# Optimization experiments

Hardware: AMD Instinct MI355X
Metric: run time of the kernel (lower is better)

Reference implementation:

```python
import jax, jax.numpy as jnp
import numpy as np

SOC, EOS = 3, 2
NUM_HEADS = 12
LN_EPS = 1e-5


def setup_inputs() -> dict:
    key = jax.random.key(0)
    ks = jax.random.split(key, 24)
    B, S, D, N, FF, K = 8, 4096, 768, 1024, 3072, 640
    img = jax.random.normal(ks[0], (B, N, D), jnp.float32)
    hid = jax.random.normal(ks[1], (B, S, D), jnp.float32)
    seq = jax.random.randint(ks[2], (B, S), 4, 100)
    m = jax.random.uniform(ks[3], (B, S)) < 0.125
    seq = jnp.where(m, SOC, seq).at[:, 0].set(SOC)  # ensure >=1 SOC per row
    w = lambda k, a, b: jax.random.normal(k, (a, b), jnp.float32) * 0.02
    return {
        "img": img, "hid": hid, "seq": seq,
        "wq_s": w(ks[4], D, D), "wk_s": w(ks[5], D, D), "wv_s": w(ks[6], D, D), "wo_s": w(ks[7], D, D),
        "wq_c": w(ks[8], D, D), "wk_c": w(ks[9], D, D), "wv_c": w(ks[10], D, D), "wo_c": w(ks[11], D, D),
        "w_ff1": w(ks[12], D, FF), "w_ff2": w(ks[13], FF, D),
        "ln1_s": jnp.ones((D,)), "ln1_b": jnp.zeros((D,)),
        "ln2_s": jnp.ones((D,)), "ln2_b": jnp.zeros((D,)),
        "ln3_s": jnp.ones((D,)), "ln3_b": jnp.zeros((D,)),
        "cap": K,
    }


def _ln(x, s, b):
    mu = jnp.mean(x, axis=-1, keepdims=True)
    var = jnp.var(x, axis=-1, keepdims=True)
    return (x - mu) * jax.lax.rsqrt(var + LN_EPS) * s + b


def _mha(q_in, kv_in, wq, wk, wv, wo, key_mask):
    # q_in [B,Lq,D], kv_in [B,Lk,D], key_mask [B,Lk] bool or None
    B, Lq, D = q_in.shape
    H = NUM_HEADS
    dh = D // H
    q = (q_in @ wq).reshape(B, Lq, H, dh)
    k = (kv_in @ wk).reshape(B, -1, H, dh)
    v = (kv_in @ wv).reshape(B, -1, H, dh)
    scores = jnp.einsum("bqhd,bkhd->bhqk", q, k) / np.sqrt(dh).astype(q.dtype)
    if key_mask is not None:
        scores = jnp.where(key_mask[:, None, None, :], scores, jnp.asarray(-1e9, scores.dtype))
    att = jax.nn.softmax(scores, axis=-1)
    out = jnp.einsum("bhqk,bkhd->bqhd", att, v).reshape(B, Lq, D)
    return out @ wo


def _extract(data, mask, cap):
    # data [B,S,...], mask [B,S] bool -> packed+zero-padded [B,cap,...]
    pos = jnp.cumsum(mask, axis=1) - 1          # slot for each valid token
    pos = jnp.where(mask, pos, cap)             # invalid tokens -> dump slot
    def one(d, p):
        buf = jnp.zeros((cap + 1,) + d.shape[1:], d.dtype)
        return buf.at[p].set(d)[:cap]
        # note: dump slot cap is sliced away
    return jax.vmap(one)(data, pos), pos


def reference(img, hid, seq, wq_s, wk_s, wv_s, wo_s, wq_c, wk_c, wv_c, wo_c,
              w_ff1, w_ff2, ln1_s, ln1_b, ln2_s, ln2_b, ln3_s, ln3_b, cap):
    # mask: SOC tokens occurring before the first EOS
    soc = (seq == SOC) & (jnp.cumsum(seq == EOS, axis=1) == 0)  # [B,S]
    ext, pos = _extract(hid, soc, cap)                          # [B,K,D]
    counts = jnp.sum(soc, axis=1)                               # [B]
    run = jnp.arange(cap)[None, :] < counts[:, None]            # [B,K] valid slots

    # Blocks: pre-LN self-attn (key mask = run), cross-attn to img, FFN
    x = ext
    x = x + _mha(_ln(x, ln1_s, ln1_b), _ln(x, ln1_s, ln1_b), wq_s, wk_s, wv_s, wo_s, run)
    x = x + _mha(_ln(x, ln2_s, ln2_b), img, wq_c, wk_c, wv_c, wo_c, None)
    h = _ln(x, ln3_s, ln3_b)
    x = x + jax.nn.gelu(h @ w_ff1) @ w_ff2

    # masked_scatter back: each SOC position (b,s) takes x[b, pos[b,s]]
    idx = jnp.clip(pos, 0, cap - 1)
    gathered = jnp.take_along_axis(x, idx[:, :, None], axis=1)  # [B,S,D]
    hid_new = jnp.where(soc[:, :, None], gathered, hid)
    return hid_new, x
```

## Files before the change

### kernel.cpp

```cpp
#include <hip/hip_runtime.h>
#include <hip/hip_bf16.h>


#define B_    8
#define S_    4096
#define D_    768
#define N_    1024
#define FF_   3072
#define H_    12
#define DH_   64
#define KCAP  640
#define SOC_TOK 3
#define EOS_TOK 2

typedef __hip_bfloat16 bf16;
typedef unsigned short u16;
typedef __attribute__((ext_vector_type(8))) short short8;
typedef __attribute__((ext_vector_type(4))) float f32x4;

__device__ __forceinline__ u16 ftou16(float x){ union{bf16 b; u16 s;} c; c.b = __float2bfloat16(x); return c.s; }
__device__ __forceinline__ unsigned pk2(float lo, float hi){ return (unsigned)ftou16(lo) | ((unsigned)ftou16(hi)<<16); }

__device__ __forceinline__ f32x4 MFMA(short8 a, short8 b, f32x4 c){
  return __builtin_amdgcn_mfma_f32_16x16x32_bf16(a, b, c, 0, 0, 0);
}

__device__ __forceinline__ void gld16(const void* gp, void* lp){
  __builtin_amdgcn_global_load_lds(
    reinterpret_cast<const __attribute__((address_space(1))) unsigned int*>((size_t)gp),
    reinterpret_cast<__attribute__((address_space(3))) unsigned int*>((size_t)lp),
    16, 0, 0);
}

template<int N> __device__ __forceinline__ void vwait(){
  asm volatile("s_waitcnt vmcnt(%0)" :: "i"(N) : "memory");
}
__device__ __forceinline__ void wgbar(){ asm volatile("s_barrier" ::: "memory"); }

__device__ __forceinline__ int xcd_swz(){
  int id = blockIdx.x;
  return (id & 7) * ((int)gridDim.x >> 3) + (id >> 3);
}

__device__ void scan_body(const int* __restrict__ seq, int* __restrict__ pos,
                          int* __restrict__ src, int* __restrict__ counts, int b){
  int tid = threadIdx.x;
  __shared__ int sd[256];
  __shared__ int carryE, carryS;
  if (tid==0){ carryE=0; carryS=0; }
  __syncthreads();
  for (int c=0; c<S_; c+=256){
    int s   = c + tid;
    int tok = seq[b*S_ + s];
    int isE = (tok==EOS_TOK) ? 1 : 0;
    int isS = (tok==SOC_TOK) ? 1 : 0;
    sd[tid]=isE; __syncthreads();
    for (int off=1; off<256; off<<=1){ int t_=(tid>=off)?sd[tid-off]:0; __syncthreads(); sd[tid]+=t_; __syncthreads(); }
    int eIncl = sd[tid];
    int eTot  = sd[255];
    int valid = (isS && (carryE + eIncl)==0) ? 1 : 0;
    __syncthreads();
    sd[tid]=valid; __syncthreads();
    for (int off=1; off<256; off<<=1){ int t_=(tid>=off)?sd[tid-off]:0; __syncthreads(); sd[tid]+=t_; __syncthreads(); }
    int vIncl = sd[tid];
    int vTot  = sd[255];
    if (valid){
      int slot = carryS + vIncl - 1;
      pos[b*S_ + s] = slot;
      if (slot < KCAP) src[b*KCAP + slot] = s;
    } else {
      pos[b*S_ + s] = -1;
    }
    __syncthreads();
    if (tid==0){ carryE += eTot; carryS += vTot; }
    __syncthreads();
  }
  if (tid==0) counts[b] = (carryS < KCAP) ? carryS : KCAP;
}

struct TransArgs { const float* w[10]; u16* o[10]; };
__global__ __launch_bounds__(256) void transpose_scan_k(TransArgs a, const int* __restrict__ seq,
                                                        int* __restrict__ pos, int* __restrict__ src,
                                                        int* __restrict__ counts,
                                                        const float* __restrict__ img, u16* __restrict__ imgB){
  int id = blockIdx.x;
  if (id >= 9224){
    int base = (id - 9224)*2048 + threadIdx.x*8;
    float4 a0 = *(const float4*)(img + base);
    float4 a1 = *(const float4*)(img + base + 4);
    uint4 wv;
    wv.x = pk2(a0.x,a0.y); wv.y = pk2(a0.z,a0.w); wv.z = pk2(a1.x,a1.y); wv.w = pk2(a1.z,a1.w);
    *(uint4*)(imgB + base) = wv;
    return;
  }
  if (id >= 9216){ scan_body(seq, pos, src, counts, id - 9216); return; }
  __shared__ float tile[32][33];
  int wi, t, K, N;
  if (id < 4608){ wi = id/576; t = id%576; K = 768; N = 768; }
  else if (id < 6912){ wi = 8; t = id-4608; K = 768; N = 3072; }
  else { wi = 9; t = id-6912; K = 3072; N = 768; }
  const float* in = a.w[wi]; u16* out = a.o[wi];
  int nbx = N >> 5;
  int bx = t % nbx, by = t / nbx;
  int tx = threadIdx.x & 31, ty = threadIdx.x >> 5;
  #pragma unroll
  for (int i=0;i<4;++i)
    tile[ty + i*8][tx] = in[(size_t)(by*32 + ty + i*8)*N + bx*32 + tx];
  __syncthreads();
  #pragma unroll
  for (int i=0;i<4;++i)
    out[(size_t)(bx*32 + ty + i*8)*K + by*32 + tx] = ftou16(tile[tx][ty + i*8]);
}

__global__ __launch_bounds__(256) void gather_ln_k(const float* __restrict__ hid,
                                                   const int* __restrict__ src,
                                                   const int* __restrict__ counts,
                                                   const float* __restrict__ g, const float* __restrict__ bt,
                                                   float* __restrict__ X, u16* __restrict__ T0){
  int bk = blockIdx.x; int b = bk / KCAP; int k = bk % KCAP;
  int tid = threadIdx.x;
  float v0, v1, v2;
  if (k < counts[b]){
    const float* hr = hid + ((size_t)b*S_ + src[b*KCAP + k])*D_;
    v0 = hr[tid]; v1 = hr[tid+256]; v2 = hr[tid+512];
  } else { v0 = v1 = v2 = 0.f; }
  float* xr = X + (size_t)bk*D_;
  xr[tid] = v0; xr[tid+256] = v1; xr[tid+512] = v2;
  float s1=v0+v1+v2, s2=v0*v0+v1*v1+v2*v2;
  for (int off=32; off; off>>=1){ s1+=__shfl_xor(s1,off); s2+=__shfl_xor(s2,off); }
  __shared__ float red[8];
  __shared__ float mu_s, rs_s;
  int w=tid>>6, ln=tid&63;
  if (ln==0){ red[w]=s1; red[4+w]=s2; }
  __syncthreads();
  if (tid==0){
    float S1=red[0]+red[1]+red[2]+red[3];
    float S2=red[4]+red[5]+red[6]+red[7];
    float mu = S1*(1.f/D_);
    float var= S2*(1.f/D_) - mu*mu;
    mu_s=mu; rs_s=rsqrtf(var + 1e-5f);
  }
  __syncthreads();
  float mu=mu_s, rs=rs_s;
  u16* yr = T0 + (size_t)bk*D_;
  yr[tid]     = ftou16((v0-mu)*rs*g[tid]     + bt[tid]);
  yr[tid+256] = ftou16((v1-mu)*rs*g[tid+256] + bt[tid+256]);
  yr[tid+512] = ftou16((v2-mu)*rs*g[tid+512] + bt[tid+512]);
}

__global__ __launch_bounds__(256) void ln_k(const float* __restrict__ X, u16* __restrict__ Y,
                                            const float* __restrict__ g, const float* __restrict__ bt){
  int r = blockIdx.x; int tid = threadIdx.x;
  const float* xr = X + (size_t)r*D_;
  float v0=xr[tid], v1=xr[tid+256], v2=xr[tid+512];
  float s1=v0+v1+v2, s2=v0*v0+v1*v1+v2*v2;
  for (int off=32; off; off>>=1){ s1+=__shfl_xor(s1,off); s2+=__shfl_xor(s2,off); }
  __shared__ float red[8];
  __shared__ float mu_s, rs_s;
  int w=tid>>6, ln=tid&63;
  if (ln==0){ red[w]=s1; red[4+w]=s2; }
  __syncthreads();
  if (tid==0){
    float S1=red[0]+red[1]+red[2]+red[3];
    float S2=red[4]+red[5]+red[6]+red[7];
    float mu = S1*(1.f/D_);
    float var= S2*(1.f/D_) - mu*mu;
    mu_s=mu; rs_s=rsqrtf(var + 1e-5f);
  }
  __syncthreads();
  float mu=mu_s, rs=rs_s;
  u16* yr = Y + (size_t)r*D_;
  yr[tid]     = ftou16((v0-mu)*rs*g[tid]     + bt[tid]);
  yr[tid+256] = ftou16((v1-mu)*rs*g[tid+256] + bt[tid+256]);
  yr[tid+512] = ftou16((v2-mu)*rs*g[tid+512] + bt[tid+512]);
}

template<int MODE, int BM, typename TA>
__device__ __forceinline__ void gemm_body(char* ldsp, const TA* __restrict__ A, const u16* __restrict__ Bt,
                                          void* __restrict__ C0, void* __restrict__ C1, void* __restrict__ C2,
                                          int wgid, int N, int K){
  constexpr int MI   = BM/32;
  constexpr int NBUF = (BM==128) ? 2 : ((sizeof(TA)==4) ? 2 : 3);
  u16* As = (u16*)ldsp;
  u16* Bs = (u16*)(ldsp + NBUF*(BM*32)*2);
  int nbx = N >> 7;
  int bx = wgid % nbx, by = wgid / nbx;
  int tid = threadIdx.x;
  int w = tid>>6, l = tid&63, g = l>>4, c = l&15;
  int wr = w&1, wc = w>>1;
  f32x4 acc[MI][4] = {};
  float4 rg[4];
  const int NK = K/32;

  auto STAGEB = [&](int buf, int kt){
    #pragma unroll
    for (int p=0;p<2;++p){
      int row = w*32 + p*16 + (l>>2);
      int su  = (l&3) ^ ((row>>1)&3);
      gld16((const void*)(Bt + (size_t)(bx*128+row)*K + kt + su*8), (void*)&Bs[buf*128*32 + (w*32+p*16)*32]);
    }
  };
  auto STAGEA16 = [&](int buf, int kt){
    if constexpr (BM==128){
      #pragma unroll
      for (int p=0;p<2;++p){
        int row = w*32 + p*16 + (l>>2);
        int su  = (l&3) ^ ((row>>1)&3);
        gld16((const void*)((const u16*)A + (size_t)(by*BM+row)*K + kt + su*8), (void*)&As[buf*BM*32 + (w*32+p*16)*32]);
      }
    } else {
      int row = w*16 + (l>>2);
      int su  = (l&3) ^ ((row>>1)&3);
      gld16((const void*)((const u16*)A + (size_t)(by*BM+row)*K + kt + su*8), (void*)&As[buf*BM*32 + (w*16)*32]);
    }
  };
  auto LOADREG = [&](int kt){
    if constexpr (BM==128){
      const float* ap = (const float*)A + (size_t)(by*BM + (tid>>1))*K + kt + (tid&1)*16;
      rg[0]=*(const float4*)ap;     rg[1]=*(const float4*)(ap+4);
      rg[2]=*(const float4*)(ap+8); rg[3]=*(const float4*)(ap+12);
    } else {
      const float* ap = (const float*)A + (size_t)(by*BM + (tid>>2))*K + kt + (tid&3)*8;
      rg[0] = *(const float4*)ap; rg[1] = *(const float4*)(ap+4);
    }
  };
  auto WRITEA = [&](int buf){
    if constexpr (BM==128){
      int row = tid>>1, half = tid&1;
      uint4 w0,w1;
      w0.x=pk2(rg[0].x,rg[0].y); w0.y=pk2(rg[0].z,rg[0].w); w0.z=pk2(rg[1].x,rg[1].y); w0.w=pk2(rg[1].z,rg[1].w);
      w1.x=pk2(rg[2].x,rg[2].y); w1.y=pk2(rg[2].z,rg[2].w); w1.z=pk2(rg[3].x,rg[3].y); w1.w=pk2(rg[3].z,rg[3].w);
      int sw = (row>>1)&3;
      *(uint4*)&As[buf*BM*32 + row*32 + ((half*2  )^sw)*8] = w0;
      *(uint4*)&As[buf*BM*32 + row*32 + ((half*2+1)^sw)*8] = w1;
    } else {
      int row = tid>>2, unit = tid&3;
      uint4 wv;
      wv.x=pk2(rg[0].x,rg[0].y); wv.y=pk2(rg[0].z,rg[0].w); wv.z=pk2(rg[1].x,rg[1].y); wv.w=pk2(rg[1].z,rg[1].w);
      int sw = (row>>1)&3;
      *(uint4*)&As[buf*BM*32 + row*32 + (unit^sw)*8] = wv;
    }
  };
  auto COMPUTE = [&](int buf){
    short8 af[MI], bfr[4];
    #pragma unroll
    for (int mi=0;mi<MI;++mi){ int row = wr*(MI*16) + mi*16 + c; af[mi]  = *(const short8*)&As[buf*BM*32 + row*32 + (g^((row>>1)&3))*8]; }
    #pragma unroll
    for (int ni=0;ni<4;++ni){ int row = wc*64 + ni*16 + c;       bfr[ni] = *(const short8*)&Bs[buf*128*32 + row*32 + (g^((row>>1)&3))*8]; }
    #pragma unroll
    for (int mi=0;mi<MI;++mi)
      #pragma unroll
      for (int ni=0;ni<4;++ni) acc[mi][ni] = MFMA(af[mi], bfr[ni], acc[mi][ni]);
  };

  if constexpr (BM==128 || sizeof(TA)==4){
    if constexpr (sizeof(TA)==4){ LOADREG(0); STAGEB(0,0); WRITEA(0); }
    else { STAGEA16(0,0); STAGEB(0,0); }
    __syncthreads();
    int buf = 0;
    for (int t=0;t<NK;++t){
      int ktn = (t+1)*32;
      if constexpr (sizeof(TA)==4){
        if (t+1<NK){ LOADREG(ktn); STAGEB(buf^1, ktn); }
        COMPUTE(buf);
        if (t+1<NK) WRITEA(buf^1);
      } else {
        if (t+1<NK){ STAGEA16(buf^1, ktn); STAGEB(buf^1, ktn); }
        COMPUTE(buf);
      }
      __syncthreads();
      buf ^= 1;
    }
  } else {
    constexpr int LPS = 3;
    STAGEA16(0,0);  STAGEB(0,0);
    STAGEA16(1,32); STAGEB(1,32);
    vwait<LPS>();
    wgbar();
    int buf = 0;
    for (int t=0;t<NK;++t){
      if (t+2 < NK){
        int nb = buf+2; if (nb>=3) nb-=3;
        STAGEA16(nb,(t+2)*32); STAGEB(nb,(t+2)*32);
      }
      COMPUTE(buf);
      if (t < NK-2) vwait<LPS>(); else vwait<0>();
      wgbar();
      ++buf; if (buf==3) buf=0;
    }
  }

  int row0 = by*BM + wr*(MI*16), col0 = bx*128 + wc*64;
  #pragma unroll
  for (int mi=0;mi<MI;++mi)
    #pragma unroll
    for (int ni=0;ni<4;++ni){
      int rowb = row0 + mi*16 + g*4;
      int col  = col0 + ni*16 + c;
      if (MODE==4 && col >= 1536){
        int vv = col - 1536; int bb = rowb / KCAP; int key = rowb - bb*KCAP;
        ushort4 pk;
        pk.x = ftou16(acc[mi][ni][0]); pk.y = ftou16(acc[mi][ni][1]);
        pk.z = ftou16(acc[mi][ni][2]); pk.w = ftou16(acc[mi][ni][3]);
        *(ushort4*)&((u16*)C2)[((size_t)(bb*768 + vv))*KCAP + key] = pk;
      } else if (MODE==5 && col >= 768){
        int vv = col - 768; int bb = rowb >> 10; int key = rowb & 1023;
        ushort4 pk;
        pk.x = ftou16(acc[mi][ni][0]); pk.y = ftou16(acc[mi][ni][1]);
        pk.z = ftou16(acc[mi][ni][2]); pk.w = ftou16(acc[mi][ni][3]);
        *(ushort4*)&((u16*)C2)[((size_t)(bb*768 + vv))*1024 + key] = pk;
      } else {
        #pragma unroll
        for (int r=0;r<4;++r){
          int row = rowb + r;
          float v = acc[mi][ni][r];
          if (MODE==0){
            ((u16*)C0)[(size_t)row*N + col] = ftou16(v);
          } else if (MODE==1){
            ((float*)C0)[(size_t)row*N + col] += v;
          } else if (MODE==2){
            float z2 = 1.5957691216057308f*(v + 0.044715f*v*v*v);
            float e  = __expf(z2);
            float th = 1.f - 2.f/(e + 1.f);
            ((u16*)C0)[(size_t)row*N + col] = ftou16(0.5f*v*(1.f+th));
          } else if (MODE==6){
            size_t idx = (size_t)row*N + col;
            float fin = ((float*)C0)[idx] + v;
            ((float*)C0)[idx] = fin;
            ((float*)C1)[idx] = fin;
          } else if (MODE==4){
            if (col < 768)  ((u16*)C0)[(size_t)row*768 + col]       = ftou16(v);
            else            ((u16*)C1)[(size_t)row*768 + col - 768] = ftou16(v);
          } else {
            ((u16*)C0)[(size_t)row*768 + col] = ftou16(v);
          }
        }
      }
    }
}

template<int MODE, int BM, typename TA>
__global__ __launch_bounds__(256) void gemm_k(const TA* __restrict__ A, const u16* __restrict__ Bt,
                                              void* __restrict__ C0, void* __restrict__ C1, void* __restrict__ C2,
                                              int N, int K){
  constexpr int NBUF = (BM==128) ? 2 : ((sizeof(TA)==4) ? 2 : 3);
  __shared__ __align__(16) char pool[NBUF*(BM+128)*32*2];
  gemm_body<MODE,BM,TA>(pool, A, Bt, C0, C1, C2, xcd_swz(), N, K);
}

__global__ __launch_bounds__(256) void mega1_k(const u16* __restrict__ T0, const u16* __restrict__ wqkv_st,
                                               u16* __restrict__ Qb, u16* __restrict__ Kb, u16* __restrict__ VtS,
                                               const u16* __restrict__ imgB, const u16* __restrict__ wkv_ct,
                                               u16* __restrict__ KbC, u16* __restrict__ VtC){
  __shared__ __align__(16) char pool[2*(128+128)*32*2];
  int wgid = xcd_swz();
  if (wgid < 720) gemm_body<4,128,u16>(pool, T0,   wqkv_st, Qb,  Kb,      VtS, wgid,     2304, 768);
  else            gemm_body<5,128,u16>(pool, imgB, wkv_ct,  KbC, nullptr, VtC, wgid-720, 1536, 768);
}

template<int MASKED>
__global__ __launch_bounds__(256) void attn_k(const u16* __restrict__ Q, const u16* __restrict__ Kb,
                                              const u16* __restrict__ Vt, u16* __restrict__ O,
                                              const int* __restrict__ counts, int Lk){
  __shared__ __align__(16) u16 Ks[3][64*64];
  __shared__ __align__(16) u16 Vs[3][64*64];
  __shared__ __align__(16) u16 P[4][16][72];
  int tid = threadIdx.x;
  int w = tid>>6, l = tid&63, g = l>>4, c = l&15;
  int wgid = xcd_swz();
  int qc = wgid % 5;
  int bh = wgid / 5;
  int h = bh % H_, b = bh / H_;
  int q0 = qc*128 + w*32;
  int cnt = MASKED ? counts[b] : Lk;
  int nt = (cnt + 63) >> 6;

  short8 qf[2][2];
  #pragma unroll
  for (int mi=0;mi<2;++mi){
    const u16* Qrow = Q + ((size_t)(b*KCAP + q0 + mi*16 + c))*D_ + h*DH_;
    qf[mi][0] = *(const short8*)(Qrow + g*8);
    qf[mi][1] = *(const short8*)(Qrow + 32 + g*8);
  }

  int srow8 = (l>>3);
  int sunit = l&7;
  auto STAGE = [&](int buf, int kb){
    #pragma unroll
    for (int p=0;p<2;++p){
      int r0 = w*16 + p*8;
      int rowK = r0 + srow8;
      int su = sunit ^ (rowK&7);
      gld16((const void*)(Kb + ((size_t)(b*Lk + kb + rowK))*D_ + h*DH_ + su*8), (void*)&Ks[buf][r0*64]);
      gld16((const void*)(Vt + ((size_t)(b*D_ + h*DH_ + rowK))*Lk + kb + su*8), (void*)&Vs[buf][r0*64]);
    }
  };

  f32x4 o[2][4] = {};
  float m_[2][4], l_[2][4] = {};
  #pragma unroll
  for (int mi=0;mi<2;++mi)
    #pragma unroll
    for (int r=0;r<4;++r) m_[mi][r] = -1e30f;

  STAGE(0, 0);
  if (nt > 1){ STAGE(1, 64); vwait<4>(); } else { vwait<0>(); }
  wgbar();
  int buf = 0;
  for (int t=0; t<nt; ++t){
    int kb = t*64;
    if (t+2 < nt){
      int nb = buf+2; if (nb>=3) nb-=3;
      STAGE(nb, kb+128);
    }
    short8 fr[4][2];
    #pragma unroll
    for (int nb=0;nb<4;++nb)
      #pragma unroll
      for (int kh=0;kh<2;++kh)
        fr[nb][kh] = *(const short8*)&Ks[buf][(nb*16+c)*64 + (((kh<<2)|g) ^ (c&7))*8];
    f32x4 z[2][4];
    #pragma unroll
    for (int mi=0;mi<2;++mi)
      #pragma unroll
      for (int nb=0;nb<4;++nb){
        f32x4 zz = {0.f,0.f,0.f,0.f};
        zz = MFMA(qf[mi][0], fr[nb][0], zz);
        zz = MFMA(qf[mi][1], fr[nb][1], zz);
        z[mi][nb] = zz;
      }
    float pv[2][4][4];
    #pragma unroll
    for (int nb=0;nb<4;++nb){
      bool msk = MASKED && (kb + nb*16 + c >= cnt);
      #pragma unroll
      for (int mi=0;mi<2;++mi)
        #pragma unroll
        for (int r=0;r<4;++r) pv[mi][nb][r] = msk ? -1e30f : z[mi][nb][r]*0.125f;
    }
    float scl[2][4];
    #pragma unroll
    for (int mi=0;mi<2;++mi){
      #pragma unroll
      for (int r=0;r<4;++r){
        float v = fmaxf(fmaxf(pv[mi][0][r],pv[mi][1][r]), fmaxf(pv[mi][2][r],pv[mi][3][r]));
        v = fmaxf(v, __shfl_xor(v,1)); v = fmaxf(v, __shfl_xor(v,2));
        v = fmaxf(v, __shfl_xor(v,4)); v = fmaxf(v, __shfl_xor(v,8));
        float nm = fmaxf(m_[mi][r], v);
        scl[mi][r] = __expf(m_[mi][r] - nm);
        m_[mi][r] = nm;
      }
      #pragma unroll
      for (int r=0;r<4;++r){
        float acc2 = 0.f;
        #pragma unroll
        for (int nb=0;nb<4;++nb){
          float e = __expf(pv[mi][nb][r] - m_[mi][r]);
          pv[mi][nb][r] = e; acc2 += e;
        }
        acc2 += __shfl_xor(acc2,1); acc2 += __shfl_xor(acc2,2);
        acc2 += __shfl_xor(acc2,4); acc2 += __shfl_xor(acc2,8);
        l_[mi][r] = l_[mi][r]*scl[mi][r] + acc2;
      }
      #pragma unroll
      for (int nbd=0;nbd<4;++nbd)
        #pragma unroll
        for (int r=0;r<4;++r) o[mi][nbd][r] *= scl[mi][r];
    }
    #pragma unroll
    for (int nbd=0;nbd<4;++nbd)
      #pragma unroll
      for (int kh=0;kh<2;++kh)
        fr[nbd][kh] = *(const short8*)&Vs[buf][(nbd*16+c)*64 + (((kh<<2)|g) ^ (c&7))*8];
    #pragma unroll
    for (int mi=0;mi<2;++mi){
      #pragma unroll
      for (int nb=0;nb<4;++nb)
        #pragma unroll
        for (int r=0;r<4;++r) P[w][g*4+r][nb*16+c] = ftou16(pv[mi][nb][r]);
      short8 pa0 = *(const short8*)&P[w][c][g*8];
      short8 pa1 = *(const short8*)&P[w][c][32 + g*8];
      #pragma unroll
      for (int nbd=0;nbd<4;++nbd){
        o[mi][nbd] = MFMA(pa0, fr[nbd][0], o[mi][nbd]);
        o[mi][nbd] = MFMA(pa1, fr[nbd][1], o[mi][nbd]);
      }
    }
    if (t < nt-2) vwait<4>(); else vwait<0>();
    wgbar();
    ++buf; if (buf==3) buf=0;
  }
  #pragma unroll
  for (int mi=0;mi<2;++mi)
    #pragma unroll
    for (int nbd=0;nbd<4;++nbd)
      #pragma unroll
      for (int r=0;r<4;++r)
        O[((size_t)(b*KCAP + q0 + mi*16 + g*4 + r))*D_ + h*DH_ + nbd*16 + c] = ftou16(o[mi][nbd][r] / l_[mi][r]);
}

__global__ __launch_bounds__(256) void scatter_k(const int* __restrict__ pos, const float* __restrict__ X,
                                                 const float* __restrict__ hid, float* __restrict__ out0){
  int bs = blockIdx.x; int tid = threadIdx.x;
  int b = bs >> 12;
  int p = pos[bs];
  float* orow = out0 + (size_t)bs*D_;
  if (p >= 0){
    int pc = p < KCAP ? p : (KCAP-1);
    const float* xr = X + ((size_t)(b*KCAP + pc))*D_;
    orow[tid]     = xr[tid];
    orow[tid+256] = xr[tid+256];
    orow[tid+512] = xr[tid+512];
  } else {
    const float* hr = hid + (size_t)bs*D_;
    orow[tid]     = hr[tid];
    orow[tid+256] = hr[tid+256];
    orow[tid+512] = hr[tid+512];
  }
}

extern "C" void kernel_launch(void* const* d_in, const int* in_sizes, int n_in,
                              void* d_out, int out_size, void* d_ws, size_t ws_size,
                              hipStream_t stream){
  const float* img  = (const float*)d_in[0];
  const float* hid  = (const float*)d_in[1];
  const int*   seq  = (const int*)  d_in[2];
  const float* W[10] = { (const float*)d_in[3], (const float*)d_in[4], (const float*)d_in[5], (const float*)d_in[6],
                         (const float*)d_in[7], (const float*)d_in[8], (const float*)d_in[9], (const float*)d_in[10],
                         (const float*)d_in[11], (const float*)d_in[12] };
  const float* ln1s = (const float*)d_in[13];
  const float* ln1b = (const float*)d_in[14];
  const float* ln2s = (const float*)d_in[15];
  const float* ln2b = (const float*)d_in[16];
  const float* ln3s = (const float*)d_in[17];
  const float* ln3b = (const float*)d_in[18];

  char* ws = (char*)d_ws;
  int*   pos    = (int*)  (ws + 0);
  int*   src    = (int*)  (ws + 131072);
  int*   counts = (int*)  (ws + 151552);
  float* X      = (float*)(ws + 151808);
  u16*   T0     = (u16*)  (ws + 15880448);
  u16*   Qb     = (u16*)  (ws + 23744768);
  u16*   Kb     = (u16*)  (ws + 31609088);
  u16*   VtS    = (u16*)  (ws + 39473408);
  u16*   KbC    = (u16*)  (ws + 47337728);
  u16*   VtC    = (u16*)  (ws + 59920640);
  u16*   AO     = (u16*)  (ws + 72503552);
  u16*   Wt     = (u16*)  (ws + 80367872);
  u16*   MID    = Qb;

  u16* wqkv_st = Wt + 0ull*589824;
  u16* wo_st   = Wt + 3ull*589824;
  u16* wq_ct   = Wt + 4ull*589824;
  u16* wkv_ct  = Wt + 5ull*589824;
  u16* wo_ct   = Wt + 7ull*589824;
  u16* wff1t   = Wt + 8ull*589824;
  u16* wff2t   = wff1t + 2359296;

  float* out0 = (float*)d_out;
  float* out1 = out0 + (size_t)B_*S_*D_;
  u16* imgB = (u16*)out1;

  TransArgs ta;
  for (int i=0;i<10;++i) ta.w[i] = W[i];
  for (int i=0;i<8;++i)  ta.o[i] = Wt + (size_t)i*589824;
  ta.o[8] = wff1t; ta.o[9] = wff2t;

  transpose_scan_k<<<12296, 256, 0, stream>>>(ta, seq, pos, src, counts, img, imgB);
  gather_ln_k<<<B_*KCAP, 256, 0, stream>>>(hid, src, counts, ln1s, ln1b, X, T0);

  const int G_MEGA1 = 720 + 768;
  const int G_N768  = (5120/64)*(768/128);
  const int G_FF1   = (5120/128)*(3072/128);
  const int G_ATT   = B_*H_*5;

  mega1_k<<<G_MEGA1, 256, 0, stream>>>(T0, wqkv_st, Qb, Kb, VtS, imgB, wkv_ct, KbC, VtC);
  attn_k<1><<<G_ATT, 256, 0, stream>>>(Qb, Kb, VtS, AO, counts, KCAP);
  gemm_k<1,64,u16><<<G_N768, 256, 0, stream>>>(AO, wo_st, X, nullptr, nullptr, 768, 768);

  ln_k<<<5120, 256, 0, stream>>>(X, T0, ln2s, ln2b);
  gemm_k<0,64,u16><<<G_N768, 256, 0, stream>>>(T0, wq_ct, Qb, nullptr, nullptr, 768, 768);
  attn_k<0><<<G_ATT, 256, 0, stream>>>(Qb, KbC, VtC, AO, counts, N_);
  gemm_k<1,64,u16><<<G_N768, 256, 0, stream>>>(AO, wo_ct, X, nullptr, nullptr, 768, 768);

  ln_k<<<5120, 256, 0, stream>>>(X, T0, ln3s, ln3b);
  gemm_k<2,128,u16><<<G_FF1, 256, 0, stream>>>(T0, wff1t, MID, nullptr, nullptr, 3072, 768);
  gemm_k<6,64,u16><<<G_N768, 256, 0, stream>>>(MID, wff2t, X, out1, nullptr, 768, 3072);

  scatter_k<<<B_*S_, 256, 0, stream>>>(pos, X, hid, out0);
}
```

Before: 427.4 us.

## Split final scatter: copy non-SOC hid rows early, scatter only SOC rows

Copying the non-SOC hidden rows into the output is moved into the early prep kernel, which runs alongside the gather+LN. The final scatter then only writes SOC rows, reading them from out1, and uses 4 rows per block. The FF2 epilogue stops writing back to X and writes only out1. The aim is to shrink the serial tail and the redundant stores. The V fragment register rename in attention is cosmetic. One risk is that the big copy now sits on the critical path earlier, since it is in the same stream, so overlap comes only within the kernel.

```diff
diff --git a/kernel.cpp b/kernel.cpp
--- a/kernel.cpp
+++ b/kernel.cpp
@@ -112,13 +112,29 @@
     out[(size_t)(bx*32 + ty + i*8)*K + by*32 + tx] = ftou16(tile[tx][ty + i*8]);
 }
 
-__global__ __launch_bounds__(256) void gather_ln_k(const float* __restrict__ hid,
-                                                   const int* __restrict__ src,
-                                                   const int* __restrict__ counts,
-                                                   const float* __restrict__ g, const float* __restrict__ bt,
-                                                   float* __restrict__ X, u16* __restrict__ T0){
-  int bk = blockIdx.x; int b = bk / KCAP; int k = bk % KCAP;
-  int tid = threadIdx.x;
+__global__ __launch_bounds__(256) void prep_k(const float* __restrict__ hid,
+                                              const int* __restrict__ src,
+                                              const int* __restrict__ counts,
+                                              const int* __restrict__ pos,
+                                              const float* __restrict__ g, const float* __restrict__ bt,
+                                              float* __restrict__ X, u16* __restrict__ T0,
+                                              float* __restrict__ out0){
+  int id = blockIdx.x; int tid = threadIdx.x;
+  if (id >= 5120){
+    int base = (id - 5120)*4;
+    #pragma unroll
+    for (int r2=0;r2<4;++r2){
+      int bs = base + r2;
+      if (pos[bs] >= 0) continue;
+      const float* hr = hid + (size_t)bs*D_;
+      float* orow = out0 + (size_t)bs*D_;
+      orow[tid]     = hr[tid];
+      orow[tid+256] = hr[tid+256];
+      orow[tid+512] = hr[tid+512];
+    }
+    return;
+  }
+  int bk = id; int b = bk / KCAP; int k = bk % KCAP;
   float v0, v1, v2;
   if (k < counts[b]){
     const float* hr = hid + ((size_t)b*S_ + src[b*KCAP + k])*D_;
@@ -325,9 +341,7 @@
             ((u16*)C0)[(size_t)row*N + col] = ftou16(0.5f*v*(1.f+th));
           } else if (MODE==6){
             size_t idx = (size_t)row*N + col;
-            float fin = ((float*)C0)[idx] + v;
-            ((float*)C0)[idx] = fin;
-            ((float*)C1)[idx] = fin;
+            ((float*)C1)[idx] = ((const float*)C0)[idx] + v;
           } else if (MODE==4){
             if (col < 768)  ((u16*)C0)[(size_t)row*768 + col]       = ftou16(v);
             else            ((u16*)C1)[(size_t)row*768 + col - 768] = ftou16(v);
@@ -467,11 +481,12 @@
         #pragma unroll
         for (int r=0;r<4;++r) o[mi][nbd][r] *= scl[mi][r];
     }
+    short8 fv[4][2];
     #pragma unroll
     for (int nbd=0;nbd<4;++nbd)
       #pragma unroll
       for (int kh=0;kh<2;++kh)
-        fr[nbd][kh] = *(const short8*)&Vs[buf][(nbd*16+c)*64 + (((kh<<2)|g) ^ (c&7))*8];
+        fv[nbd][kh] = *(const short8*)&Vs[buf][(nbd*16+c)*64 + (((kh<<2)|g) ^ (c&7))*8];
     #pragma unroll
     for (int mi=0;mi<2;++mi){
       #pragma unroll
@@ -482,8 +497,8 @@
       short8 pa1 = *(const short8*)&P[w][c][32 + g*8];
       #pragma unroll
       for (int nbd=0;nbd<4;++nbd){
-        o[mi][nbd] = MFMA(pa0, fr[nbd][0], o[mi][nbd]);
-        o[mi][nbd] = MFMA(pa1, fr[nbd][1], o[mi][nbd]);
+        o[mi][nbd] = MFMA(pa0, fv[nbd][0], o[mi][nbd]);
+        o[mi][nbd] = MFMA(pa1, fv[nbd][1], o[mi][nbd]);
       }
     }
     if (t < nt-2) vwait<4>(); else vwait<0>();
@@ -499,23 +514,22 @@
         O[((size_t)(b*KCAP + q0 + mi*16 + g*4 + r))*D_ + h*DH_ + nbd*16 + c] = ftou16(o[mi][nbd][r] / l_[mi][r]);
 }
 
-__global__ __launch_bounds__(256) void scatter_k(const int* __restrict__ pos, const float* __restrict__ X,
-                                                 const float* __restrict__ hid, float* __restrict__ out0){
-  int bs = blockIdx.x; int tid = threadIdx.x;
-  int b = bs >> 12;
-  int p = pos[bs];
-  float* orow = out0 + (size_t)bs*D_;
-  if (p >= 0){
+__global__ __launch_bounds__(256) void scatter_soc_k(const int* __restrict__ pos,
+                                                     const float* __restrict__ out1,
+                                                     float* __restrict__ out0){
+  int base = blockIdx.x*4; int tid = threadIdx.x;
+  #pragma unroll
+  for (int r2=0;r2<4;++r2){
+    int bs = base + r2;
+    int p = pos[bs];
+    if (p < 0) continue;
     int pc = p < KCAP ? p : (KCAP-1);
-    const float* xr = X + ((size_t)(b*KCAP + pc))*D_;
+    int b = bs >> 12;
+    const float* xr = out1 + ((size_t)(b*KCAP + pc))*D_;
+    float* orow = out0 + (size_t)bs*D_;
     orow[tid]     = xr[tid];
     orow[tid+256] = xr[tid+256];
     orow[tid+512] = xr[tid+512];
-  } else {
-    const float* hr = hid + (size_t)bs*D_;
-    orow[tid]     = hr[tid];
-    orow[tid+256] = hr[tid+256];
-    orow[tid+512] = hr[tid+512];
   }
 }
 
@@ -568,7 +582,7 @@
   ta.o[8] = wff1t; ta.o[9] = wff2t;
 
   transpose_scan_k<<<12296, 256, 0, stream>>>(ta, seq, pos, src, counts, img, imgB);
-  gather_ln_k<<<B_*KCAP, 256, 0, stream>>>(hid, src, counts, ln1s, ln1b, X, T0);
+  prep_k<<<13312, 256, 0, stream>>>(hid, src, counts, pos, ln1s, ln1b, X, T0, out0);
 
   const int G_MEGA1 = 720 + 768;
   const int G_N768  = (5120/64)*(768/128);
@@ -588,5 +602,5 @@
   gemm_k<2,128,u16><<<G_FF1, 256, 0, stream>>>(T0, wff1t, MID, nullptr, nullptr, 3072, 768);
   gemm_k<6,64,u16><<<G_N768, 256, 0, stream>>>(MID, wff2t, X, out1, nullptr, 768, 3072);
 
-  scatter_k<<<B_*S_, 256, 0, stream>>>(pos, X, hid, out0);
-}
+  scatter_soc_k<<<8192, 256, 0, stream>>>(pos, out1, out0);
+}
```

New measurement: 413.3 us. 1.03x faster.
